# Performance work log

Hardware: AMD Instinct MI355X
Metric: run time of the kernel (lower is better)

Reference implementation:

```python
import jax, jax.numpy as jnp
import numpy as np

EPS = 1e-8


def setup_inputs() -> dict:
    key = jax.random.key(0)
    k1, k2, k3, k4 = jax.random.split(key, 4)
    B, N, M, C = 512, 512, 128, 1024
    addr = M + 6  # read head: k(M) + beta(1) + g(1) + s(3) + gamma(1)
    controller_out = jax.random.normal(k1, (B, C), dtype=jnp.float32)
    prev_w = jax.random.uniform(k2, (B, N), dtype=jnp.float32)
    prev_w = prev_w / prev_w.sum(axis=1, keepdims=True)  # valid weighting
    memory_state = jax.random.normal(k3, (B, N, M), dtype=jnp.float32)
    W_fc = jax.random.normal(k4, (C, addr), dtype=jnp.float32) * 0.02
    b_fc = jnp.zeros((addr,), dtype=jnp.float32)
    return {"controller_out": controller_out, "prev_w": prev_w,
            "memory_state": memory_state, "W_fc": W_fc, "b_fc": b_fc}


def reference(controller_out, prev_w, memory_state, W_fc, b_fc):
    M = memory_state.shape[2]
    out = controller_out @ W_fc + b_fc  # [B, M+6]
    k = out[:, :M]                                   # key
    beta = jax.nn.softplus(out[:, M:M + 1])          # key strength
    g = jax.nn.sigmoid(out[:, M + 1:M + 2])          # interpolation gate
    s = jax.nn.softmax(out[:, M + 2:M + 5], axis=1)  # 3-tap shift weights
    gamma = 1.0 + jax.nn.softplus(out[:, M + 5:M + 6])

    # Content addressing (Eq. 5-6): cosine similarity + sharpened softmax
    norm_k = jnp.linalg.norm(k, axis=1, keepdims=True) + EPS      # [B,1]
    norm_mem = jnp.linalg.norm(memory_state, axis=2) + EPS        # [B,N]
    sim = jnp.einsum('bnm,bm->bn', memory_state, k) / (norm_k * norm_mem)
    w_c = jax.nn.softmax(beta * sim, axis=1)

    # Interpolation (Eq. 7)
    w_g = g * w_c + (1.0 - g) * prev_w

    # Circular 3-tap shift (Eq. 8): vectorized roll instead of per-slot loop
    w_s = (s[:, 0:1] * jnp.roll(w_g, 1, axis=1)
           + s[:, 1:2] * w_g
           + s[:, 2:3] * jnp.roll(w_g, -1, axis=1))

    # Sharpening (Eq. 9)
    w_pow = w_s ** gamma
    w = w_pow / (w_pow.sum(axis=1, keepdims=True) + EPS)

    # Read vector (read head)
    read_vec = jnp.einsum('bn,bnm->bm', w, memory_state)
    return (read_vec, w)
```

## Files before the change

### kernel.cpp

```cpp
#include <hip/hip_runtime.h>
#include <math.h>

#define BB   512
#define NN   512
#define MM   128
#define CC   1024
#define ADDR 134
#define EPSF 1e-8f

__device__ __forceinline__ float softplus_f(float x) {
    return fmaxf(x, 0.0f) + log1pf(expf(-fabsf(x)));
}

__global__ __launch_bounds__(256) void ntm_head_kernel(
    const float* __restrict__ co,
    const float* __restrict__ prev_w,
    const float* __restrict__ mem,
    const float* __restrict__ W_fc,
    const float* __restrict__ b_fc,
    float* __restrict__ out_rv,
    float* __restrict__ out_w)
{
    __shared__ __align__(16) float s_co[CC];
    __shared__ __align__(16) float s_k[MM];
    __shared__ float s_extra[8];
    __shared__ float s_bsim[NN];
    __shared__ float s_wg[NN];
    __shared__ float s_w[NN];
    __shared__ __align__(16) float s_part[8 * MM];
    __shared__ float s_red[8];
    __shared__ float s_params[8];

    const int t = threadIdx.x;
    const int b = blockIdx.x;

    for (int c = t; c < CC; c += 256) s_co[c] = co[(size_t)b * CC + c];
    __syncthreads();

    if (t < ADDR) {
        float a0 = 0.f, a1 = 0.f, a2 = 0.f, a3 = 0.f;
        const float* Wp = W_fc + t;
        for (int c = 0; c < CC; c += 4) {
            float4 cv = *(const float4*)(s_co + c);
            a0 = fmaf(cv.x, Wp[(size_t)(c + 0) * ADDR], a0);
            a1 = fmaf(cv.y, Wp[(size_t)(c + 1) * ADDR], a1);
            a2 = fmaf(cv.z, Wp[(size_t)(c + 2) * ADDR], a2);
            a3 = fmaf(cv.w, Wp[(size_t)(c + 3) * ADDR], a3);
        }
        float r = ((a0 + a1) + (a2 + a3)) + b_fc[t];
        if (t < MM) s_k[t] = r; else s_extra[t - MM] = r;
    }
    __syncthreads();

    {
        float v = (t < MM) ? s_k[t] * s_k[t] : 0.0f;
        #pragma unroll
        for (int off = 32; off >= 1; off >>= 1) v += __shfl_xor(v, off, 64);
        if ((t & 63) == 0) s_red[t >> 6] = v;
        __syncthreads();
        if (t == 0) {
            float ks = s_red[0] + s_red[1] + s_red[2] + s_red[3];
            float norm_k = sqrtf(ks) + EPSF;
            float beta = softplus_f(s_extra[0]);
            float g = 1.0f / (1.0f + expf(-s_extra[1]));
            float e0 = s_extra[2], e1 = s_extra[3], e2 = s_extra[4];
            float mx = fmaxf(e0, fmaxf(e1, e2));
            float x0 = expf(e0 - mx), x1 = expf(e1 - mx), x2 = expf(e2 - mx);
            float inv = 1.0f / (x0 + x1 + x2);
            s_params[0] = beta / norm_k;
            s_params[1] = g;
            s_params[2] = x0 * inv;
            s_params[3] = x1 * inv;
            s_params[4] = x2 * inv;
            s_params[5] = 1.0f + softplus_f(s_extra[5]);
        }
    }
    __syncthreads();

    const float bnk = s_params[0];
    const float4* memb = (const float4*)(mem + (size_t)b * NN * MM);

    {
        const int gi = t >> 5;
        const int l  = t & 31;
        float4 kv = ((const float4*)s_k)[l];
        for (int n0 = gi; n0 < NN; n0 += 32) {
            float4 a0 = memb[(size_t)(n0     ) * 32 + l];
            float4 a1 = memb[(size_t)(n0 +  8) * 32 + l];
            float4 a2 = memb[(size_t)(n0 + 16) * 32 + l];
            float4 a3 = memb[(size_t)(n0 + 24) * 32 + l];
            float d0 = a0.x*kv.x + a0.y*kv.y + a0.z*kv.z + a0.w*kv.w;
            float q0 = a0.x*a0.x + a0.y*a0.y + a0.z*a0.z + a0.w*a0.w;
            float d1 = a1.x*kv.x + a1.y*kv.y + a1.z*kv.z + a1.w*kv.w;
            float q1 = a1.x*a1.x + a1.y*a1.y + a1.z*a1.z + a1.w*a1.w;
            float d2 = a2.x*kv.x + a2.y*kv.y + a2.z*kv.z + a2.w*kv.w;
            float q2 = a2.x*a2.x + a2.y*a2.y + a2.z*a2.z + a2.w*a2.w;
            float d3 = a3.x*kv.x + a3.y*kv.y + a3.z*kv.z + a3.w*kv.w;
            float q3 = a3.x*a3.x + a3.y*a3.y + a3.z*a3.z + a3.w*a3.w;
            #pragma unroll
            for (int off = 16; off >= 1; off >>= 1) {
                d0 += __shfl_xor(d0, off, 64); q0 += __shfl_xor(q0, off, 64);
                d1 += __shfl_xor(d1, off, 64); q1 += __shfl_xor(q1, off, 64);
                d2 += __shfl_xor(d2, off, 64); q2 += __shfl_xor(q2, off, 64);
                d3 += __shfl_xor(d3, off, 64); q3 += __shfl_xor(q3, off, 64);
            }
            if (l == 0) {
                s_bsim[n0     ] = bnk * d0 / (sqrtf(q0) + EPSF);
                s_bsim[n0 +  8] = bnk * d1 / (sqrtf(q1) + EPSF);
                s_bsim[n0 + 16] = bnk * d2 / (sqrtf(q2) + EPSF);
                s_bsim[n0 + 24] = bnk * d3 / (sqrtf(q3) + EPSF);
            }
        }
    }
    __syncthreads();

    {
        const int n1 = t, n2 = t + 256;
        float b1 = s_bsim[n1], b2 = s_bsim[n2];

        float m = fmaxf(b1, b2);
        #pragma unroll
        for (int off = 32; off >= 1; off >>= 1) m = fmaxf(m, __shfl_xor(m, off, 64));
        if ((t & 63) == 0) s_red[t >> 6] = m;
        __syncthreads();
        float M4 = fmaxf(fmaxf(s_red[0], s_red[1]), fmaxf(s_red[2], s_red[3]));
        __syncthreads();

        float e1 = expf(b1 - M4), e2 = expf(b2 - M4);
        float ls = e1 + e2;
        #pragma unroll
        for (int off = 32; off >= 1; off >>= 1) ls += __shfl_xor(ls, off, 64);
        if ((t & 63) == 0) s_red[t >> 6] = ls;
        __syncthreads();
        float S = s_red[0] + s_red[1] + s_red[2] + s_red[3];
        __syncthreads();

        const float invS = 1.0f / S;
        const float g = s_params[1];
        float wg1 = fmaf(g, e1 * invS, (1.0f - g) * prev_w[(size_t)b * NN + n1]);
        float wg2 = fmaf(g, e2 * invS, (1.0f - g) * prev_w[(size_t)b * NN + n2]);
        s_wg[n1] = wg1;
        s_wg[n2] = wg2;
        __syncthreads();

        const float sh0 = s_params[2], sh1 = s_params[3], sh2 = s_params[4];
        const float gamma = s_params[5];
        float ws1 = sh0 * s_wg[(n1 + NN - 1) & (NN - 1)] + sh1 * wg1 + sh2 * s_wg[(n1 + 1) & (NN - 1)];
        float ws2 = sh0 * s_wg[(n2 + NN - 1) & (NN - 1)] + sh1 * wg2 + sh2 * s_wg[(n2 + 1) & (NN - 1)];
        float wp1 = powf(ws1, gamma);
        float wp2 = powf(ws2, gamma);

        float lz = wp1 + wp2;
        #pragma unroll
        for (int off = 32; off >= 1; off >>= 1) lz += __shfl_xor(lz, off, 64);
        if ((t & 63) == 0) s_red[t >> 6] = lz;
        __syncthreads();
        float Z = s_red[0] + s_red[1] + s_red[2] + s_red[3];
        __syncthreads();

        const float invZ = 1.0f / (Z + EPSF);
        float w1 = wp1 * invZ, w2 = wp2 * invZ;
        s_w[n1] = w1;
        s_w[n2] = w2;
        out_w[(size_t)b * NN + n1] = w1;
        out_w[(size_t)b * NN + n2] = w2;
    }
    __syncthreads();

    {
        const int q = t >> 5;
        const int l = t & 31;
        float4 acc = make_float4(0.f, 0.f, 0.f, 0.f);
        const int nb = q * 64;
        for (int n = nb; n < nb + 64; n += 4) {
            float4 a0 = memb[(size_t)(n    ) * 32 + l];
            float4 a1 = memb[(size_t)(n + 1) * 32 + l];
            float4 a2 = memb[(size_t)(n + 2) * 32 + l];
            float4 a3 = memb[(size_t)(n + 3) * 32 + l];
            float w0 = s_w[n], w1 = s_w[n + 1], w2 = s_w[n + 2], w3 = s_w[n + 3];
            acc.x = fmaf(w0, a0.x, acc.x); acc.y = fmaf(w0, a0.y, acc.y);
            acc.z = fmaf(w0, a0.z, acc.z); acc.w = fmaf(w0, a0.w, acc.w);
            acc.x = fmaf(w1, a1.x, acc.x); acc.y = fmaf(w1, a1.y, acc.y);
            acc.z = fmaf(w1, a1.z, acc.z); acc.w = fmaf(w1, a1.w, acc.w);
            acc.x = fmaf(w2, a2.x, acc.x); acc.y = fmaf(w2, a2.y, acc.y);
            acc.z = fmaf(w2, a2.z, acc.z); acc.w = fmaf(w2, a2.w, acc.w);
            acc.x = fmaf(w3, a3.x, acc.x); acc.y = fmaf(w3, a3.y, acc.y);
            acc.z = fmaf(w3, a3.z, acc.z); acc.w = fmaf(w3, a3.w, acc.w);
        }
        *((float4*)&s_part[q * MM + l * 4]) = acc;
        __syncthreads();
        if (t < MM) {
            float r = 0.f;
            #pragma unroll
            for (int q2 = 0; q2 < 8; ++q2) r += s_part[q2 * MM + t];
            out_rv[(size_t)b * MM + t] = r;
        }
    }
}

extern "C" void kernel_launch(void* const* d_in, const int* in_sizes, int n_in,
                              void* d_out, int out_size, void* d_ws, size_t ws_size,
                              hipStream_t stream) {
    const float* co     = (const float*)d_in[0];
    const float* prev_w = (const float*)d_in[1];
    const float* mem    = (const float*)d_in[2];
    const float* W_fc   = (const float*)d_in[3];
    const float* b_fc   = (const float*)d_in[4];
    float* out = (float*)d_out;
    ntm_head_kernel<<<BB, 256, 0, stream>>>(co, prev_w, mem, W_fc, b_fc,
                                            out, out + (size_t)BB * MM);
}
```

Baseline: 239.5 us.

## Use 1024-thread blocks and split FC projection across all threads

Raises the block size from 256 to 1024 threads so each batch row is processed by four times as many threads. The controller projection, previously done serially by 134 threads over the full 1024-long input, is now split into eight partial sums per key output, with each of the six scalar head outputs reduced by a dedicated wave. Memory passes spread 512 rows over 32 groups, and the read-vector reduction becomes a two-level shared-memory sum. This adds more barriers and more shared memory per block, and a 1024-thread block may lower occupancy per CU.

```diff
diff --git a/kernel.cpp b/kernel.cpp
--- a/kernel.cpp
+++ b/kernel.cpp
@@ -1,5 +1,6 @@
 #include <hip/hip_runtime.h>
 #include <math.h>
+#include <float.h>
 
 #define BB   512
 #define NN   512
@@ -12,7 +13,7 @@
     return fmaxf(x, 0.0f) + log1pf(expf(-fabsf(x)));
 }
 
-__global__ __launch_bounds__(256) void ntm_head_kernel(
+__global__ __launch_bounds__(1024, 8) void ntm_head_kernel(
     const float* __restrict__ co,
     const float* __restrict__ prev_w,
     const float* __restrict__ mem,
@@ -24,71 +25,98 @@
     __shared__ __align__(16) float s_co[CC];
     __shared__ __align__(16) float s_k[MM];
     __shared__ float s_extra[8];
-    __shared__ float s_bsim[NN];
+    __shared__ __align__(16) float s_bsim[NN];
     __shared__ float s_wg[NN];
     __shared__ float s_w[NN];
-    __shared__ __align__(16) float s_part[8 * MM];
-    __shared__ float s_red[8];
+    __shared__ __align__(16) float s_part[32 * MM];
+    __shared__ float s_red[16];
     __shared__ float s_params[8];
 
     const int t = threadIdx.x;
     const int b = blockIdx.x;
 
-    for (int c = t; c < CC; c += 256) s_co[c] = co[(size_t)b * CC + c];
-    __syncthreads();
-
-    if (t < ADDR) {
+    s_co[t] = co[(size_t)b * CC + t];
+
+    float pw = 0.0f;
+    if (t < NN) pw = prev_w[(size_t)b * NN + t];
+
+    __syncthreads();
+
+    {
+        const int o    = t & (MM - 1);
+        const int part = t >> 7;
+        const float* Wp = W_fc + o;
         float a0 = 0.f, a1 = 0.f, a2 = 0.f, a3 = 0.f;
-        const float* Wp = W_fc + t;
-        for (int c = 0; c < CC; c += 4) {
+        const int c0 = part * (CC / 8);
+        for (int c = c0; c < c0 + CC / 8; c += 4) {
             float4 cv = *(const float4*)(s_co + c);
             a0 = fmaf(cv.x, Wp[(size_t)(c + 0) * ADDR], a0);
             a1 = fmaf(cv.y, Wp[(size_t)(c + 1) * ADDR], a1);
             a2 = fmaf(cv.z, Wp[(size_t)(c + 2) * ADDR], a2);
             a3 = fmaf(cv.w, Wp[(size_t)(c + 3) * ADDR], a3);
         }
-        float r = ((a0 + a1) + (a2 + a3)) + b_fc[t];
-        if (t < MM) s_k[t] = r; else s_extra[t - MM] = r;
-    }
-    __syncthreads();
-
-    {
-        float v = (t < MM) ? s_k[t] * s_k[t] : 0.0f;
+        s_part[part * MM + o] = (a0 + a1) + (a2 + a3);
+
+        const int wv = t >> 6;
+        if (wv < 6) {
+            const int l  = t & 63;
+            const int oe = MM + wv;
+            const float* We = W_fc + oe;
+            float e = 0.f;
+            for (int c = l; c < CC; c += 64)
+                e = fmaf(s_co[c], We[(size_t)c * ADDR], e);
+            #pragma unroll
+            for (int off = 32; off >= 1; off >>= 1) e += __shfl_xor(e, off, 64);
+            if (l == 0) s_extra[wv] = e + b_fc[oe];
+        }
+    }
+    __syncthreads();
+
+    if (t < MM) {
+        float r = b_fc[t];
+        #pragma unroll
+        for (int p = 0; p < 8; ++p) r += s_part[p * MM + t];
+        s_k[t] = r;
+        float v = r * r;
         #pragma unroll
         for (int off = 32; off >= 1; off >>= 1) v += __shfl_xor(v, off, 64);
         if ((t & 63) == 0) s_red[t >> 6] = v;
-        __syncthreads();
-        if (t == 0) {
-            float ks = s_red[0] + s_red[1] + s_red[2] + s_red[3];
-            float norm_k = sqrtf(ks) + EPSF;
-            float beta = softplus_f(s_extra[0]);
-            float g = 1.0f / (1.0f + expf(-s_extra[1]));
-            float e0 = s_extra[2], e1 = s_extra[3], e2 = s_extra[4];
-            float mx = fmaxf(e0, fmaxf(e1, e2));
-            float x0 = expf(e0 - mx), x1 = expf(e1 - mx), x2 = expf(e2 - mx);
-            float inv = 1.0f / (x0 + x1 + x2);
-            s_params[0] = beta / norm_k;
-            s_params[1] = g;
-            s_params[2] = x0 * inv;
-            s_params[3] = x1 * inv;
-            s_params[4] = x2 * inv;
-            s_params[5] = 1.0f + softplus_f(s_extra[5]);
-        }
+    }
+    __syncthreads();
+    if (t == 0) {
+        float ks = s_red[0] + s_red[1];
+        float norm_k = sqrtf(ks) + EPSF;
+        float beta = softplus_f(s_extra[0]);
+        float g = 1.0f / (1.0f + expf(-s_extra[1]));
+        float e0 = s_extra[2], e1 = s_extra[3], e2 = s_extra[4];
+        float mx = fmaxf(e0, fmaxf(e1, e2));
+        float x0 = expf(e0 - mx), x1 = expf(e1 - mx), x2 = expf(e2 - mx);
+        float inv = 1.0f / (x0 + x1 + x2);
+        s_params[0] = beta / norm_k;
+        s_params[1] = g;
+        s_params[2] = x0 * inv;
+        s_params[3] = x1 * inv;
+        s_params[4] = x2 * inv;
+        s_params[5] = 1.0f + softplus_f(s_extra[5]);
     }
     __syncthreads();
 
     const float bnk = s_params[0];
     const float4* memb = (const float4*)(mem + (size_t)b * NN * MM);
-
-    {
-        const int gi = t >> 5;
-        const int l  = t & 31;
+    const int gi = t >> 5;
+    const int l  = t & 31;
+
+    {
         float4 kv = ((const float4*)s_k)[l];
-        for (int n0 = gi; n0 < NN; n0 += 32) {
-            float4 a0 = memb[(size_t)(n0     ) * 32 + l];
-            float4 a1 = memb[(size_t)(n0 +  8) * 32 + l];
-            float4 a2 = memb[(size_t)(n0 + 16) * 32 + l];
-            float4 a3 = memb[(size_t)(n0 + 24) * 32 + l];
+        for (int j = 0; j < 16; j += 4) {
+            const int r0 = gi + (j    ) * 32;
+            const int r1 = gi + (j + 1) * 32;
+            const int r2 = gi + (j + 2) * 32;
+            const int r3 = gi + (j + 3) * 32;
+            float4 a0 = memb[r0 * 32 + l];
+            float4 a1 = memb[r1 * 32 + l];
+            float4 a2 = memb[r2 * 32 + l];
+            float4 a3 = memb[r3 * 32 + l];
             float d0 = a0.x*kv.x + a0.y*kv.y + a0.z*kv.z + a0.w*kv.w;
             float q0 = a0.x*a0.x + a0.y*a0.y + a0.z*a0.z + a0.w*a0.w;
             float d1 = a1.x*kv.x + a1.y*kv.y + a1.z*kv.z + a1.w*kv.w;
@@ -105,79 +133,86 @@
                 d3 += __shfl_xor(d3, off, 64); q3 += __shfl_xor(q3, off, 64);
             }
             if (l == 0) {
-                s_bsim[n0     ] = bnk * d0 / (sqrtf(q0) + EPSF);
-                s_bsim[n0 +  8] = bnk * d1 / (sqrtf(q1) + EPSF);
-                s_bsim[n0 + 16] = bnk * d2 / (sqrtf(q2) + EPSF);
-                s_bsim[n0 + 24] = bnk * d3 / (sqrtf(q3) + EPSF);
+                s_bsim[r0] = bnk * d0 / (sqrtf(q0) + EPSF);
+                s_bsim[r1] = bnk * d1 / (sqrtf(q1) + EPSF);
+                s_bsim[r2] = bnk * d2 / (sqrtf(q2) + EPSF);
+                s_bsim[r3] = bnk * d3 / (sqrtf(q3) + EPSF);
             }
         }
     }
     __syncthreads();
 
     {
-        const int n1 = t, n2 = t + 256;
-        float b1 = s_bsim[n1], b2 = s_bsim[n2];
-
-        float m = fmaxf(b1, b2);
+        const float NEG = -3.0e38f;
+        float b1 = (t < NN) ? s_bsim[t] : NEG;
+
+        float m = b1;
         #pragma unroll
         for (int off = 32; off >= 1; off >>= 1) m = fmaxf(m, __shfl_xor(m, off, 64));
         if ((t & 63) == 0) s_red[t >> 6] = m;
         __syncthreads();
-        float M4 = fmaxf(fmaxf(s_red[0], s_red[1]), fmaxf(s_red[2], s_red[3]));
-        __syncthreads();
-
-        float e1 = expf(b1 - M4), e2 = expf(b2 - M4);
-        float ls = e1 + e2;
+        float M8 = s_red[0];
+        #pragma unroll
+        for (int i = 1; i < 8; ++i) M8 = fmaxf(M8, s_red[i]);
+        __syncthreads();
+
+        float e1 = (t < NN) ? expf(b1 - M8) : 0.0f;
+        float ls = e1;
         #pragma unroll
         for (int off = 32; off >= 1; off >>= 1) ls += __shfl_xor(ls, off, 64);
         if ((t & 63) == 0) s_red[t >> 6] = ls;
         __syncthreads();
-        float S = s_red[0] + s_red[1] + s_red[2] + s_red[3];
+        float S = s_red[0];
+        #pragma unroll
+        for (int i = 1; i < 8; ++i) S += s_red[i];
         __syncthreads();
 
         const float invS = 1.0f / S;
         const float g = s_params[1];
-        float wg1 = fmaf(g, e1 * invS, (1.0f - g) * prev_w[(size_t)b * NN + n1]);
-        float wg2 = fmaf(g, e2 * invS, (1.0f - g) * prev_w[(size_t)b * NN + n2]);
-        s_wg[n1] = wg1;
-        s_wg[n2] = wg2;
+        float wg1 = fmaf(g, e1 * invS, (1.0f - g) * pw);
+        if (t < NN) s_wg[t] = wg1;
         __syncthreads();
 
         const float sh0 = s_params[2], sh1 = s_params[3], sh2 = s_params[4];
         const float gamma = s_params[5];
-        float ws1 = sh0 * s_wg[(n1 + NN - 1) & (NN - 1)] + sh1 * wg1 + sh2 * s_wg[(n1 + 1) & (NN - 1)];
-        float ws2 = sh0 * s_wg[(n2 + NN - 1) & (NN - 1)] + sh1 * wg2 + sh2 * s_wg[(n2 + 1) & (NN - 1)];
-        float wp1 = powf(ws1, gamma);
-        float wp2 = powf(ws2, gamma);
-
-        float lz = wp1 + wp2;
+        float wp1 = 0.0f;
+        if (t < NN) {
+            float ws1 = sh0 * s_wg[(t + NN - 1) & (NN - 1)]
+                      + sh1 * wg1
+                      + sh2 * s_wg[(t + 1) & (NN - 1)];
+            wp1 = powf(ws1, gamma);
+        }
+        float lz = wp1;
         #pragma unroll
         for (int off = 32; off >= 1; off >>= 1) lz += __shfl_xor(lz, off, 64);
         if ((t & 63) == 0) s_red[t >> 6] = lz;
         __syncthreads();
-        float Z = s_red[0] + s_red[1] + s_red[2] + s_red[3];
+        float Z = s_red[0];
+        #pragma unroll
+        for (int i = 1; i < 8; ++i) Z += s_red[i];
         __syncthreads();
 
         const float invZ = 1.0f / (Z + EPSF);
-        float w1 = wp1 * invZ, w2 = wp2 * invZ;
-        s_w[n1] = w1;
-        s_w[n2] = w2;
-        out_w[(size_t)b * NN + n1] = w1;
-        out_w[(size_t)b * NN + n2] = w2;
-    }
-    __syncthreads();
-
-    {
-        const int q = t >> 5;
-        const int l = t & 31;
+        if (t < NN) {
+            float w1 = wp1 * invZ;
+            s_w[t] = w1;
+            out_w[(size_t)b * NN + t] = w1;
+        }
+    }
+    __syncthreads();
+
+    {
         float4 acc = make_float4(0.f, 0.f, 0.f, 0.f);
-        const int nb = q * 64;
-        for (int n = nb; n < nb + 64; n += 4) {
-            float4 a0 = memb[(size_t)(n    ) * 32 + l];
-            float4 a1 = memb[(size_t)(n + 1) * 32 + l];
-            float4 a2 = memb[(size_t)(n + 2) * 32 + l];
-            float4 a3 = memb[(size_t)(n + 3) * 32 + l];
-            float w0 = s_w[n], w1 = s_w[n + 1], w2 = s_w[n + 2], w3 = s_w[n + 3];
+        for (int j = 0; j < 16; j += 4) {
+            const int r0 = gi + (j    ) * 32;
+            const int r1 = gi + (j + 1) * 32;
+            const int r2 = gi + (j + 2) * 32;
+            const int r3 = gi + (j + 3) * 32;
+            float4 a0 = memb[r0 * 32 + l];
+            float4 a1 = memb[r1 * 32 + l];
+            float4 a2 = memb[r2 * 32 + l];
+            float4 a3 = memb[r3 * 32 + l];
+            float w0 = s_w[r0], w1 = s_w[r1], w2 = s_w[r2], w3 = s_w[r3];
             acc.x = fmaf(w0, a0.x, acc.x); acc.y = fmaf(w0, a0.y, acc.y);
             acc.z = fmaf(w0, a0.z, acc.z); acc.w = fmaf(w0, a0.w, acc.w);
             acc.x = fmaf(w1, a1.x, acc.x); acc.y = fmaf(w1, a1.y, acc.y);
@@ -187,12 +222,20 @@
             acc.x = fmaf(w3, a3.x, acc.x); acc.y = fmaf(w3, a3.y, acc.y);
             acc.z = fmaf(w3, a3.z, acc.z); acc.w = fmaf(w3, a3.w, acc.w);
         }
-        *((float4*)&s_part[q * MM + l * 4]) = acc;
-        __syncthreads();
-        if (t < MM) {
+        *((float4*)&s_part[gi * MM + l * 4]) = acc;
+        __syncthreads();
+
+        if (t < 512) {
+            const int h = t >> 7;
+            const int o = t & (MM - 1);
             float r = 0.f;
             #pragma unroll
-            for (int q2 = 0; q2 < 8; ++q2) r += s_part[q2 * MM + t];
+            for (int q = 0; q < 8; ++q) r += s_part[(h * 8 + q) * MM + o];
+            s_bsim[h * MM + o] = r;
+        }
+        __syncthreads();
+        if (t < MM) {
+            float r = s_bsim[t] + s_bsim[MM + t] + s_bsim[2 * MM + t] + s_bsim[3 * MM + t];
             out_rv[(size_t)b * MM + t] = r;
         }
     }
@@ -207,6 +250,6 @@
     const float* W_fc   = (const float*)d_in[3];
     const float* b_fc   = (const float*)d_in[4];
     float* out = (float*)d_out;
-    ntm_head_kernel<<<BB, 256, 0, stream>>>(co, prev_w, mem, W_fc, b_fc,
-                                            out, out + (size_t)BB * MM);
+    ntm_head_kernel<<<BB, 1024, 0, stream>>>(co, prev_w, mem, W_fc, b_fc,
+                                             out, out + (size_t)BB * MM);
 }
```

Result: faster. 227.6 us (-5.0%).
